# Optimization experiments

Hardware: AMD Instinct MI355X
Metric: run time of the kernel (lower is better)

## Reference

```python
import jax, jax.numpy as jnp
import numpy as np

MEAN = 0.1307
SIGMA = 0.3081
BINARY_ITER = 10
SIG_SCALE = 5.0


def spu(x):
    # SPU(x) = x^2 - 0.5 for x >= 0, sigmoid(-x) - 1 for x < 0 (continuous at 0)
    return jnp.where(x >= 0, x * x - 0.5, jax.nn.sigmoid(-x) - 1.0)


def joining_line(x1, y1, x2, y2):
    slope = (y2 - y1) / (x2 - x1)
    return slope, y2 - slope * x2


def parabola_tangent(x):
    return 2.0 * x, -x * x - 0.5


def parabola_tangent_through(x1, y1):
    D = 4.0 * x1 * x1 - 4.0 * y1 - 2.0
    x2 = (2.0 * x1 + jnp.sqrt(jnp.clip(D, 0.0))) / 2.0
    return parabola_tangent(x2)


def sigmoid_tangent(x):
    s = jax.nn.sigmoid(x)
    slope = -s * (1.0 - s)
    return slope, -s - slope * x


def binary_search_point(lx, ux, uy):
    L = lx
    R = jnp.zeros_like(lx)
    for _ in range(BINARY_ITER):  # fixed 10-iteration search, unrolled
        m = 0.5 * (L + R)
        sm, im = sigmoid_tangent(m)
        mask = sm * ux + im - uy > 0
        L = jnp.where(mask, m, L)
        R = jnp.where(mask, R, m)
    return L


def line_to_constraint(slope, intercept):
    # [n, n+1]: diagonal slope matrix with intercept as last column (matches torch diagflat/cat)
    return jnp.concatenate([jnp.diagflat(slope), intercept[:, None]], axis=1)


def analyze_affine(W, b, ub, lb):
    constr = jnp.concatenate([W, b[:, None]], axis=1)
    bu = jnp.where(W > 0, ub[None, :], lb[None, :])
    bl = jnp.where(W > 0, lb[None, :], ub[None, :])
    return constr, jnp.einsum('ij,ij->i', bu, W) + b, jnp.einsum('ij,ij->i', bl, W) + b


def analyze_spu(ux, lx):
    uy = spu(ux)
    ly = spu(lx)
    new_ub = jnp.maximum(uy, ly)
    sj, ij = joining_line(lx, ly, ux, uy)
    right = lx > 0
    left = ux <= 0
    crossing = (~left) & (~right)
    # learned positions at their (fresh) init: sigmoid(0) -> midpoint
    mid = 0.5 * (ux + lx)
    sp, ip = parabola_tangent(mid)
    ssm, ism = sigmoid_tangent(mid)
    new_lb = jnp.where(crossing, jnp.full_like(uy, -0.5), jnp.minimum(uy, ly))
    # crossing-case lower constraint
    spu_, ipu = parabola_tangent(ux)
    limit = spu_ * lx + ipu
    clm = (jnp.abs(lx) > ux).astype(lx.dtype)
    clp = jax.nn.sigmoid((clm - 0.5) * 2.0 * SIG_SCALE) * (ly - limit) + limit
    ptm = clp < -0.5
    spt, ipt = parabola_tangent_through(lx, clp)
    sjn, ijn = joining_line(lx, clp, jnp.zeros_like(lx), jnp.full_like(lx, -0.5))
    s_cl = jnp.where(ptm, spt, sjn)
    i_cl = jnp.where(ptm, ipt, ijn)
    # crossing-case upper constraint
    ssl, isl = sigmoid_tangent(lx)
    stv = ssl * ux + isl - uy
    L = binary_search_point(lx, ux, uy)
    scp = jax.nn.sigmoid(-SIG_SCALE) * (L - lx) + lx
    ssc, isc = sigmoid_tangent(scp)
    up_mask = stv > 0
    s_cu = jnp.where(up_mask, ssc, sj)
    i_cu = jnp.where(up_mask, isc, ij)
    rf = right.astype(lx.dtype)
    lf = left.astype(lx.dtype)
    cf = crossing.astype(lx.dtype)
    us = rf * sj + lf * ssm + cf * s_cu
    ui = rf * ij + lf * ism + cf * i_cu
    ls = rf * sp + lf * sj + cf * s_cl
    li = rf * ip + lf * ij + cf * i_cl
    return line_to_constraint(us, ui), line_to_constraint(ls, li), new_ub, new_lb


def back_substitute(uc, lc, ub, lb):
    cu, cl = uc[-1], lc[-1]
    for pu, pl in zip(uc[-2::-1], lc[-2::-1]):
        # where(curr>0, prev_upper, prev_lower) contracted with curr == split pos/neg matmuls
        Wu, bu = cu[:, :-1], cu[:, -1]
        cu = jnp.maximum(Wu, 0.0) @ pu + jnp.minimum(Wu, 0.0) @ pl
        cu = cu.at[:, -1].add(bu)
        Wl, bl = cl[:, :-1], cl[:, -1]
        cl = jnp.maximum(Wl, 0.0) @ pl + jnp.minimum(Wl, 0.0) @ pu
        cl = cl.at[:, -1].add(bl)
    return jnp.minimum(ub, cu[:, 0]), jnp.maximum(lb, cl[:, 0])


def setup_inputs() -> dict:
    key = jax.random.key(0)
    ks = jax.random.split(key, 9)
    d_in, h, d_out = 784, 2048, 10
    inputs = jax.random.uniform(ks[0], (d_in,), dtype=jnp.float32)
    eps = jnp.float32(0.05)
    w1 = jax.random.normal(ks[1], (h, d_in), dtype=jnp.float32) / np.sqrt(d_in).astype(np.float32)
    b1 = jax.random.normal(ks[2], (h,), dtype=jnp.float32) * 0.1
    w2 = jax.random.normal(ks[3], (h, h), dtype=jnp.float32) / np.sqrt(h).astype(np.float32)
    b2 = jax.random.normal(ks[4], (h,), dtype=jnp.float32) * 0.1
    w3 = jax.random.normal(ks[5], (h, h), dtype=jnp.float32) / np.sqrt(h).astype(np.float32)
    b3 = jax.random.normal(ks[6], (h,), dtype=jnp.float32) * 0.1
    w4 = jax.random.normal(ks[7], (d_out, h), dtype=jnp.float32) / np.sqrt(h).astype(np.float32)
    b4 = jax.random.normal(ks[8], (d_out,), dtype=jnp.float32) * 0.1
    return {"inputs": inputs, "eps": eps, "w1": w1, "b1": b1, "w2": w2, "b2": b2,
            "w3": w3, "b3": b3, "w4": w4, "b4": b4}


def reference(inputs, eps, w1, b1, w2, b2, w3, b3, w4, b4):
    ub = [jnp.clip(inputs + eps, None, 1.0)]
    lb = [jnp.clip(inputs - eps, 0.0)]
    # normalization layer: applied in place to bounds and input constraint ([784,1])
    uc = [((ub[0] - MEAN) / SIGMA)[:, None]]
    lc = [((lb[0] - MEAN) / SIGMA)[:, None]]
    ub[0] = (ub[0] - MEAN) / SIGMA
    lb[0] = (lb[0] - MEAN) / SIGMA
    weights = [(w1, b1), (w2, b2), (w3, b3), (w4, b4)]
    for i, (W, b) in enumerate(weights):
        c, u, l = analyze_affine(W, b, ub[-1], lb[-1])
        uc.append(c)
        lc.append(c)
        ub.append(u)
        lb.append(l)
        u, l = back_substitute(uc, lc, ub[-1], lb[-1])
        ub[-1], lb[-1] = u, l
        if i < len(weights) - 1:
            cu_, cl_, u, l = analyze_spu(ub[-1], lb[-1])
            uc.append(cu_)
            lc.append(cl_)
            ub.append(u)
            lb.append(l)
            u, l = back_substitute(uc, lc, ub[-1], lb[-1])
            ub[-1], lb[-1] = u, l
    return lb[-1].min()
```

## Files before the change

### kernel.cpp

```cpp
#include <hip/hip_runtime.h>
#include <cstdint>
#include <cstddef>

#define MEAN_C 0.1307f
#define SIGMA_C 0.3081f
#define SIG_SCALE_C 5.0f

typedef __bf16 bf16_t;
typedef __bf16 bf16x8 __attribute__((ext_vector_type(8)));
typedef __bf16 bf16x4 __attribute__((ext_vector_type(4)));
typedef float f32x4 __attribute__((ext_vector_type(4)));

__device__ __forceinline__ f32x4 mfma16(bf16x8 a, bf16x8 b, f32x4 c) {
    return __builtin_amdgcn_mfma_f32_16x16x32_bf16(a, b, c, 0, 0, 0);
}

typedef const __attribute__((address_space(1))) void* gvp;
typedef __attribute__((address_space(3))) void* lvp;
__device__ __forceinline__ void g2l16(const void* g, void* l) {
    __builtin_amdgcn_global_load_lds((gvp)g, (lvp)l, 16, 0, 0);
}

__device__ __forceinline__ size_t swz(int r, int k, int ktiles) {
    return (((size_t)(r >> 4) * ktiles + (k >> 5)) << 9)
         + (((k >> 3) & 3) << 7) + ((r & 15) << 3) + (k & 7);
}

#define KTILES 64


__device__ __forceinline__ float sigmoidf_(float x) {
    if (x >= 0.f) { float e = __expf(-x); return 1.f / (1.f + e); }
    float e = __expf(x); return e / (1.f + e);
}

__device__ __forceinline__ float spu_f(float x) {
    return (x >= 0.f) ? (x * x - 0.5f) : (sigmoidf_(-x) - 1.f);
}

__device__ __forceinline__ float wave_sum(float a) {
    #pragma unroll
    for (int o = 32; o > 0; o >>= 1) a += __shfl_xor(a, o, 64);
    return a;
}

__device__ __forceinline__ void spu_body(int i, int n,
        float iUi, float iLi, float vU, float vL,
        float* __restrict__ us, float* __restrict__ ui,
        float* __restrict__ ls, float* __restrict__ li,
        float* __restrict__ pU, float* __restrict__ pL) {
    float ux = fminf(iUi, vU);
    float lx = fmaxf(iLi, vL);
    float uy = spu_f(ux), ly = spu_f(lx);
    float new_ub = fmaxf(uy, ly);
    float sj = (uy - ly) / (ux - lx);
    float ij = uy - sj * ux;
    bool right = lx > 0.f;
    bool left = ux <= 0.f;
    float mid = 0.5f * (ux + lx);
    float sp = 2.f * mid, ip = -mid * mid - 0.5f;
    float sm = sigmoidf_(mid);
    float ssm = -sm * (1.f - sm);
    float ism = -sm - ssm * mid;
    bool crossing = (!left) && (!right);
    float new_lb = crossing ? -0.5f : fminf(uy, ly);
    float spu_s = 2.f * ux, ipu = -ux * ux - 0.5f;
    float limit = spu_s * lx + ipu;
    float clm = (fabsf(lx) > ux) ? 1.f : 0.f;
    float clp = sigmoidf_((clm - 0.5f) * 2.f * SIG_SCALE_C) * (ly - limit) + limit;
    bool ptm = clp < -0.5f;
    float D = 4.f * lx * lx - 4.f * clp - 2.f;
    float x2 = (2.f * lx + sqrtf(fmaxf(D, 0.f))) * 0.5f;
    float spt = 2.f * x2, ipt = -x2 * x2 - 0.5f;
    float sjn = (clp + 0.5f) / lx;
    float ijn = -0.5f;
    float s_cl = ptm ? spt : sjn;
    float i_cl = ptm ? ipt : ijn;
    float sl = sigmoidf_(lx);
    float ssl = -sl * (1.f - sl);
    float isl = -sl - ssl * lx;
    float stv = ssl * ux + isl - uy;
    float Lb = lx, Rb = 0.f;
    #pragma unroll
    for (int t = 0; t < 10; ++t) {
        float mm = 0.5f * (Lb + Rb);
        float smm = sigmoidf_(mm);
        float sms = -smm * (1.f - smm);
        float smi = -smm - sms * mm;
        bool mask = (sms * ux + smi - uy) > 0.f;
        Lb = mask ? mm : Lb;
        Rb = mask ? Rb : mm;
    }
    float scp = sigmoidf_(-SIG_SCALE_C) * (Lb - lx) + lx;
    float sc = sigmoidf_(scp);
    float ssc = -sc * (1.f - sc);
    float isc = -sc - ssc * scp;
    bool up = stv > 0.f;
    float s_cu = up ? ssc : sj;
    float i_cu = up ? isc : ij;
    float usv, uiv, lsv, liv;
    if (right)      { usv = sj;   uiv = ij;   lsv = sp;   liv = ip;   }
    else if (left)  { usv = ssm;  uiv = ism;  lsv = sj;   liv = ij;   }
    else            { usv = s_cu; uiv = i_cu; lsv = s_cl; liv = i_cl; }
    us[i] = usv; ui[i] = uiv; ls[i] = lsv; li[i] = liv;
    float vu = (usv >= 0.f) ? vU : vL;
    float vl = (lsv >= 0.f) ? vL : vU;
    pU[i] = fminf(new_ub, usv * vu + uiv);
    pL[i] = fmaxf(new_lb, lsv * vl + liv);
}


__global__ __launch_bounds__(256) void k_interval_spu(
        const float* __restrict__ W, const float* __restrict__ b,
        const float* __restrict__ U, const float* __restrict__ L,
        int m, int n,
        float* __restrict__ us, float* __restrict__ ui,
        float* __restrict__ ls, float* __restrict__ li,
        float* __restrict__ pU, float* __restrict__ pL) {
    int r = (blockIdx.x << 2) + (threadIdx.x >> 6);
    if (r >= n) return;
    int lane = threadIdx.x & 63;
    const f32x4* Wr = (const f32x4*)(W + (size_t)r * m);
    const f32x4* U4 = (const f32x4*)U;
    const f32x4* L4 = (const f32x4*)L;
    int nf4 = m >> 2;
    float au = 0.f, al = 0.f;
    for (int j = lane; j < nf4; j += 64) {
        f32x4 wv = Wr[j], uu = U4[j], ll = L4[j];
        #pragma unroll
        for (int u = 0; u < 4; ++u) {
            float w = wv[u];
            float hi = (w > 0.f) ? uu[u] : ll[u];
            float lo2 = (w > 0.f) ? ll[u] : uu[u];
            au = fmaf(w, hi, au);
            al = fmaf(w, lo2, al);
        }
    }
    au = wave_sum(au); al = wave_sum(al);
    if (lane == 0) {
        float vU = au + b[r], vL = al + b[r];
        spu_body(r, n, vU, vL, vU, vL, us, ui, ls, li, pU, pL);
    }
}

__global__ void k_spu2(const float* __restrict__ iU, const float* __restrict__ iL,
                       const float* __restrict__ vraw, int n,
                       float* __restrict__ us, float* __restrict__ ui,
                       float* __restrict__ ls, float* __restrict__ li,
                       float* __restrict__ pU, float* __restrict__ pL) {
    int i = blockIdx.x * blockDim.x + threadIdx.x;
    if (i >= n) return;
    spu_body(i, n, iU[i], iL[i], vraw[i], vraw[n + i], us, ui, ls, li, pU, pL);
}


__global__ __launch_bounds__(256) void k_wT3(
        const float* __restrict__ W1, const float* __restrict__ W2,
        const float* __restrict__ W3,
        bf16_t* __restrict__ W1t, bf16_t* __restrict__ W2t, bf16_t* __restrict__ W3t,
        const float* __restrict__ x, const float* __restrict__ eps,
        float* __restrict__ ubn, float* __restrict__ lbn) {
    __shared__ bf16_t t[64 * 65];
    int z = blockIdx.z;
    const float* W; int N, ldw; bf16_t* Wt;
    if (z == 0)      { W = W2; N = 2048; ldw = 2048; Wt = W2t; }
    else if (z == 1) { W = W3; N = 2048; ldw = 2048; Wt = W3t; }
    else {
        W = W1; N = 784; ldw = 784; Wt = W1t;
        if (blockIdx.y >= 14) {
            if (blockIdx.y == 14 && blockIdx.x == 0) {
                for (int i = threadIdx.x; i < 896; i += 256) {
                    if (i >= 784) { ubn[i] = 0.f; lbn[i] = 0.f; }
                    else {
                        float e = eps[0];
                        float ub = fminf(x[i] + e, 1.f);
                        float lb = fmaxf(x[i] - e, 0.f);
                        ubn[i] = (ub - MEAN_C) / SIGMA_C;
                        lbn[i] = (lb - MEAN_C) / SIGMA_C;
                    }
                }
            }
            return;
        }
    }
    int k0 = blockIdx.x * 64, n0 = blockIdx.y * 64;
    int tid = threadIdx.x;
    int rg = tid >> 4;
    int cg = (tid & 15) * 4;
    bool fast = (n0 + 64 <= N);
    #pragma unroll
    for (int it = 0; it < 4; ++it) {
        int row = it * 16 + rg;
        const float* Wr = W + (size_t)(k0 + row) * ldw + n0 + cg;
        float v0, v1, v2, v3;
        if (fast) {
            f32x4 vv = *(const f32x4*)Wr;
            v0 = vv[0]; v1 = vv[1]; v2 = vv[2]; v3 = vv[3];
        } else {
            v0 = (n0 + cg + 0 < N) ? Wr[0] : 0.f;
            v1 = (n0 + cg + 1 < N) ? Wr[1] : 0.f;
            v2 = (n0 + cg + 2 < N) ? Wr[2] : 0.f;
            v3 = (n0 + cg + 3 < N) ? Wr[3] : 0.f;
        }
        t[(cg + 0) * 65 + row] = (bf16_t)v0;
        t[(cg + 1) * 65 + row] = (bf16_t)v1;
        t[(cg + 2) * 65 + row] = (bf16_t)v2;
        t[(cg + 3) * 65 + row] = (bf16_t)v3;
    }
    __syncthreads();
    #pragma unroll
    for (int p = 0; p < 2; ++p) {
        int c = tid + p * 256;
        int lr = c & 63, lq = c >> 6;
        bf16x8 v;
        #pragma unroll
        for (int u = 0; u < 8; ++u) v[u] = t[lr * 65 + lq * 8 + u];
        *(bf16x8*)(Wt + swz(n0 + lr, k0 + lq * 8, KTILES)) = v;
    }
}

__global__ __launch_bounds__(256) void k_prep16(
        const float* __restrict__ W, const float* __restrict__ b, int n,
        const float* __restrict__ cus, const float* __restrict__ cui,
        const float* __restrict__ cls, const float* __restrict__ cli,
        const float* __restrict__ bvec,
        const float* __restrict__ U, const float* __restrict__ L,
        bf16_t* __restrict__ Ab, float* __restrict__ av,
        float* __restrict__ iU, float* __restrict__ iL) {
    int rt = blockIdx.x;
    int tid = threadIdx.x, lane = tid & 63, wid = tid >> 6;
    int mrow = lane & 15, q = lane >> 4;
    int r = rt * 16 + mrow;
    bool act = r < 2 * n;
    bool isU = r < n;
    int i = act ? (isU ? r : r - n) : 0;
    float gate = act ? 1.f : 0.f;
    const float* Wr = W + (size_t)i * 2048;
    const float* ps = isU ? cus : cls;
    const float* ns = isU ? cls : cus;
    const float* yi = isU ? cui : cli;
    const float* zi = isU ? cli : cui;
    const float* hi = isU ? U : L;
    const float* lo = isU ? L : U;
    float a = 0.f, a2 = 0.f;
    bf16_t* Abase = Ab + ((size_t)rt * KTILES) * 512 + lane * 8;
    for (int kt = wid; kt < KTILES; kt += 4) {
        int k0 = kt * 32 + q * 8;
        bf16x8 ov;
        #pragma unroll
        for (int h = 0; h < 2; ++h) {
            int kb = k0 + 4 * h;
            f32x4 wv = *(const f32x4*)(Wr + kb);
            f32x4 p0 = *(const f32x4*)(ps + kb);
            f32x4 q0 = *(const f32x4*)(ns + kb);
            f32x4 y0 = *(const f32x4*)(yi + kb);
            f32x4 z0 = *(const f32x4*)(zi + kb);
            f32x4 c0 = *(const f32x4*)(bvec + kb);
            f32x4 h0 = *(const f32x4*)(hi + kb);
            f32x4 l0 = *(const f32x4*)(lo + kb);
            #pragma unroll
            for (int u = 0; u < 4; ++u) {
                float w = gate * wv[u];
                float pos = fmaxf(w, 0.f), neg = fminf(w, 0.f);
                float mx = pos * p0[u] + neg * q0[u];
                ov[4 * h + u] = (bf16_t)mx;
                a += pos * y0[u] + neg * z0[u] + mx * c0[u];
                a2 += pos * h0[u] + neg * l0[u];
            }
        }
        *(bf16x8*)(Abase + (size_t)kt * 512) = ov;
    }
    a += __shfl_xor(a, 16, 64);  a += __shfl_xor(a, 32, 64);
    a2 += __shfl_xor(a2, 16, 64); a2 += __shfl_xor(a2, 32, 64);
    __shared__ float sh[2][4][16];
    if (lane < 16) { sh[0][wid][lane] = a; sh[1][wid][lane] = a2; }
    __syncthreads();
    if (tid < 16) {
        int r2 = rt * 16 + tid;
        float ta = sh[0][0][tid] + sh[0][1][tid] + sh[0][2][tid] + sh[0][3][tid];
        float tb = sh[1][0][tid] + sh[1][1][tid] + sh[1][2][tid] + sh[1][3][tid];
        if (r2 < 2 * n) {
            bool isU2 = r2 < n;
            int i2 = isU2 ? r2 : r2 - n;
            av[r2] = ta + b[i2];
            if (isU2) iU[i2] = tb + b[i2];
            else      iL[i2] = tb + b[i2];
        } else {
            av[r2] = 0.f;
        }
    }
}

__global__ __launch_bounds__(256) void k_colmix16(
        const bf16_t* __restrict__ Cb, int ldc, int splits, size_t sstride, int n,
        int tpb,
        const float* __restrict__ cus, const float* __restrict__ cui,
        const float* __restrict__ cls, const float* __restrict__ cli,
        const float* __restrict__ bvec,
        bf16_t* __restrict__ Ab, float* __restrict__ av) {
    int rt = blockIdx.x;
    int kt0 = blockIdx.y * tpb;
    int tid = threadIdx.x, lane = tid & 63, wid = tid >> 6;
    int mrow = lane & 15, q = lane >> 4;
    int r = rt * 16 + mrow;
    bool isU = r < n;
    const bf16_t* Cr = Cb + (size_t)r * ldc;
    const float* ps = isU ? cus : cls;
    const float* ns = isU ? cls : cus;
    const float* yi = isU ? cui : cli;
    const float* zi = isU ? cli : cui;
    float a = 0.f;
    bf16_t* Abase = Ab + ((size_t)rt * KTILES) * 512 + lane * 8;
    for (int kt = kt0 + wid; kt < kt0 + tpb; kt += 4) {
        int k0 = kt * 32 + q * 8;
        float wsum[8] = {0.f, 0.f, 0.f, 0.f, 0.f, 0.f, 0.f, 0.f};
        for (int s = 0; s < splits; ++s) {
            bf16x8 v = *(const bf16x8*)(Cr + s * sstride + k0);
            #pragma unroll
            for (int u = 0; u < 8; ++u) wsum[u] += (float)v[u];
        }
        f32x4 p0 = *(const f32x4*)(ps + k0), p1 = *(const f32x4*)(ps + k0 + 4);
        f32x4 q0 = *(const f32x4*)(ns + k0), q1 = *(const f32x4*)(ns + k0 + 4);
        f32x4 y0 = *(const f32x4*)(yi + k0), y1 = *(const f32x4*)(yi + k0 + 4);
        f32x4 z0 = *(const f32x4*)(zi + k0), z1 = *(const f32x4*)(zi + k0 + 4);
        f32x4 c0 = *(const f32x4*)(bvec + k0), c1 = *(const f32x4*)(bvec + k0 + 4);
        bf16x8 ov;
        #pragma unroll
        for (int u = 0; u < 4; ++u) {
            float w = wsum[u];
            float pos = fmaxf(w, 0.f), neg = fminf(w, 0.f);
            float mx = pos * p0[u] + neg * q0[u];
            ov[u] = (bf16_t)mx;
            a += pos * y0[u] + neg * z0[u] + mx * c0[u];
        }
        #pragma unroll
        for (int u = 0; u < 4; ++u) {
            float w = wsum[4 + u];
            float pos = fmaxf(w, 0.f), neg = fminf(w, 0.f);
            float mx = pos * p1[u] + neg * q1[u];
            ov[4 + u] = (bf16_t)mx;
            a += pos * y1[u] + neg * z1[u] + mx * c1[u];
        }
        *(bf16x8*)(Abase + (size_t)kt * 512) = ov;
    }
    a += __shfl_xor(a, 16, 64);
    a += __shfl_xor(a, 32, 64);
    __shared__ float sh[4][16];
    if (lane < 16) sh[wid][lane] = a;
    __syncthreads();
    if (tid < 16) {
        float tot = sh[0][tid] + sh[1][tid] + sh[2][tid] + sh[3][tid];
        atomicAdd(&av[rt * 16 + tid], tot);
    }
}

__global__ __launch_bounds__(640) void k_reduce16f(
        const bf16_t* __restrict__ Cb, int ldc, int m, int n,
        int splits, size_t sstride,
        const float* __restrict__ av,
        const float* __restrict__ ubn, const float* __restrict__ lbn,
        const float* __restrict__ iL,
        float* __restrict__ out) {
    __shared__ float sbl[16];
    int tid = threadIdx.x, lane = tid & 63, wv = tid >> 6;
    int nch = m >> 3;
    int i = wv;
    int r = n + i;
    const bf16_t* Cr = Cb + (size_t)r * ldc;
    const float* p = lbn;
    const float* q = ubn;
    float a = 0.f;
    for (int c = lane; c < nch; c += 64) {
        float wsum[8] = {0.f, 0.f, 0.f, 0.f, 0.f, 0.f, 0.f, 0.f};
        for (int s = 0; s < splits; ++s) {
            bf16x8 v = *(const bf16x8*)(Cr + s * sstride + c * 8);
            #pragma unroll
            for (int u = 0; u < 8; ++u) wsum[u] += (float)v[u];
        }
        f32x4 p0 = *(const f32x4*)(p + c * 8), p1 = *(const f32x4*)(p + c * 8 + 4);
        f32x4 q0 = *(const f32x4*)(q + c * 8), q1 = *(const f32x4*)(q + c * 8 + 4);
        #pragma unroll
        for (int u = 0; u < 4; ++u) {
            a += fmaxf(wsum[u], 0.f) * p0[u] + fminf(wsum[u], 0.f) * q0[u];
            a += fmaxf(wsum[4 + u], 0.f) * p1[u] + fminf(wsum[4 + u], 0.f) * q1[u];
        }
    }
    a = wave_sum(a);
    if (lane == 0) sbl[i] = fmaxf(iL[i], a + av[r]);
    __syncthreads();
    if (tid < 64) {
        float v = 3.4e38f;
        for (int j = lane; j < n; j += 64) v = fminf(v, sbl[j]);
        #pragma unroll
        for (int o = 32; o > 0; o >>= 1) v = fminf(v, __shfl_down(v, o, 64));
        if (lane == 0) out[0] = v;
    }
}

#define GEMM_PIPE()                                                            \
    int tid = threadIdx.x, lane = tid & 63, w = tid >> 6;                      \
    int wm = w & 1, wn = w >> 1;                                               \
    f32x4 acc[4][4];                                                           \
    _Pragma("unroll")                                                          \
    for (int i = 0; i < 4; ++i)                                                \
        _Pragma("unroll")                                                      \
        for (int j = 0; j < 4; ++j) acc[i][j] = (f32x4){0.f, 0.f, 0.f, 0.f};   \
    auto stage = [&](int kk) {                                                 \
        int b = kk & 1;                                                        \
        size_t go = (size_t)kk * 1024;                                         \
        bf16_t* la = &As2[b * 8192 + w * 1024];                                \
        bf16_t* lb = &Bs2[b * 8192 + w * 1024];                                \
        g2l16(a0 + go, la);          g2l16(a0 + go + 512, la + 512);           \
        g2l16(a1 + go, la + 4096);   g2l16(a1 + go + 512, la + 4608);          \
        g2l16(b0 + go, lb);          g2l16(b0 + go + 512, lb + 512);           \
        g2l16(b1 + go, lb + 4096);   g2l16(b1 + go + 512, lb + 4608);          \
    };                                                                         \
    stage(0); stage(1);                                                        \
    asm volatile("s_waitcnt vmcnt(8)" ::: "memory");                           \
    __builtin_amdgcn_s_barrier();                                              \
    for (int kk = 0; kk < nk; ++kk) {                                          \
        const bf16_t* cA = &As2[(kk & 1) * 8192];                              \
        const bf16_t* cB = &Bs2[(kk & 1) * 8192];                              \
        bf16x8 af0[4], af1[4], bq0[4], bq1[4];                                 \
        _Pragma("unroll")                                                      \
        for (int i = 0; i < 4; ++i) {                                          \
            af0[i] = *(const bf16x8*)(cA + (wm * 4 + i) * 1024 + lane * 8);    \
            af1[i] = *(const bf16x8*)(cA + (wm * 4 + i) * 1024 + 512 + lane * 8); \
            bq0[i] = *(const bf16x8*)(cB + (wn * 4 + i) * 1024 + lane * 8);    \
            bq1[i] = *(const bf16x8*)(cB + (wn * 4 + i) * 1024 + 512 + lane * 8); \
        }                                                                      \
        asm volatile("s_waitcnt lgkmcnt(0)" ::: "memory");                     \
        __builtin_amdgcn_s_barrier();                                          \
        if (kk + 2 < nk) stage(kk + 2);                                        \
        _Pragma("unroll")                                                      \
        for (int i = 0; i < 4; ++i)                                            \
            _Pragma("unroll")                                                  \
            for (int j = 0; j < 4; ++j)                                        \
                acc[i][j] = mfma16(bq0[j], af0[i], acc[i][j]);                 \
        _Pragma("unroll")                                                      \
        for (int i = 0; i < 4; ++i)                                            \
            _Pragma("unroll")                                                  \
            for (int j = 0; j < 4; ++j)                                        \
                acc[i][j] = mfma16(bq1[j], af1[i], acc[i][j]);                 \
        if (kk + 2 < nk) asm volatile("s_waitcnt vmcnt(8)" ::: "memory");      \
        else             asm volatile("s_waitcnt vmcnt(0)" ::: "memory");      \
        __builtin_amdgcn_s_barrier();                                          \
    }

__global__ __launch_bounds__(256) void k_gemm16(
        const bf16_t* __restrict__ A, const bf16_t* __restrict__ Bt,
        bf16_t* __restrict__ C, int ldc, size_t sstride, int nk) {
    __shared__ __align__(16) bf16_t As2[16384];
    __shared__ __align__(16) bf16_t Bs2[16384];
    int tr0 = blockIdx.y * 8, tc0 = blockIdx.x * 8;
    int kt0 = blockIdx.z * nk * 2;
    int wtmp = threadIdx.x >> 6, ltmp = threadIdx.x & 63;
    const bf16_t* a0 = A + (((size_t)(tr0 + wtmp)     * KTILES + kt0) << 9) + ltmp * 8;
    const bf16_t* a1 = A + (((size_t)(tr0 + wtmp + 4) * KTILES + kt0) << 9) + ltmp * 8;
    const bf16_t* b0 = Bt + (((size_t)(tc0 + wtmp)     * KTILES + kt0) << 9) + ltmp * 8;
    const bf16_t* b1 = Bt + (((size_t)(tc0 + wtmp + 4) * KTILES + kt0) << 9) + ltmp * 8;
    GEMM_PIPE()
    bf16_t* Cz = C + (size_t)blockIdx.z * sstride;
    int orow = lane & 15, ocol = (lane >> 4) * 4;
    size_t row0 = (size_t)blockIdx.y * 128;
    size_t col0 = (size_t)blockIdx.x * 128;
    #pragma unroll
    for (int i = 0; i < 4; ++i) {
        size_t gr = row0 + wm * 64 + i * 16 + orow;
        #pragma unroll
        for (int j = 0; j < 4; ++j) {
            size_t gc = col0 + wn * 64 + j * 16 + ocol;
            bf16x4 v;
            #pragma unroll
            for (int rg = 0; rg < 4; ++rg) v[rg] = (bf16_t)acc[i][j][rg];
            *(bf16x4*)(Cz + gr * (size_t)ldc + gc) = v;
        }
    }
}

#define GEMM_PIPE8()                                                           \
    int tid = threadIdx.x, lane = tid & 63, w = tid >> 6;            \
    int wm = w >> 2, wn = w & 3;                                               \
    f32x4 acc[4][2];                                                           \
    _Pragma("unroll")                                                          \
    for (int i = 0; i < 4; ++i)                                                \
        _Pragma("unroll")                                                      \
        for (int j = 0; j < 2; ++j) acc[i][j] = (f32x4){0.f, 0.f, 0.f, 0.f};   \
    auto stage = [&](int kk) {                                                 \
        int b = kk & 1;                                                        \
        size_t go = (size_t)kk * 1024;                                         \
        bf16_t* la = &As2[b * 8192 + w * 1024];                                \
        bf16_t* lb = &Bs2[b * 8192 + w * 1024];                                \
        g2l16(a0 + go, la);   g2l16(a0 + go + 512, la + 512);                  \
        g2l16(b0 + go, lb);   g2l16(b0 + go + 512, lb + 512);                  \
    };                                                                         \
    stage(0); stage(1);                                                        \
    asm volatile("s_waitcnt vmcnt(4)" ::: "memory");                           \
    __builtin_amdgcn_s_barrier();                                              \
    for (int kk = 0; kk < nk; ++kk) {                                          \
        const bf16_t* cA = &As2[(kk & 1) * 8192];                              \
        const bf16_t* cB = &Bs2[(kk & 1) * 8192];                              \
        bf16x8 af0[4], af1[4], bq0[2], bq1[2];                                 \
        _Pragma("unroll")                                                      \
        for (int i = 0; i < 4; ++i) {                                          \
            af0[i] = *(const bf16x8*)(cA + (wm * 4 + i) * 1024 + lane * 8);    \
            af1[i] = *(const bf16x8*)(cA + (wm * 4 + i) * 1024 + 512 + lane * 8); \
        }                                                                      \
        _Pragma("unroll")                                                      \
        for (int j = 0; j < 2; ++j) {                                          \
            bq0[j] = *(const bf16x8*)(cB + (wn * 2 + j) * 1024 + lane * 8);    \
            bq1[j] = *(const bf16x8*)(cB + (wn * 2 + j) * 1024 + 512 + lane * 8); \
        }                                                                      \
        asm volatile("s_waitcnt lgkmcnt(0)" ::: "memory");                     \
        __builtin_amdgcn_s_barrier();                                          \
        if (kk + 2 < nk) stage(kk + 2);                                        \
        _Pragma("unroll")                                                      \
        for (int i = 0; i < 4; ++i)                                            \
            _Pragma("unroll")                                                  \
            for (int j = 0; j < 2; ++j)                                        \
                acc[i][j] = mfma16(bq0[j], af0[i], acc[i][j]);                 \
        _Pragma("unroll")                                                      \
        for (int i = 0; i < 4; ++i)                                            \
            _Pragma("unroll")                                                  \
            for (int j = 0; j < 2; ++j)                                        \
                acc[i][j] = mfma16(bq1[j], af1[i], acc[i][j]);                 \
        if (kk + 2 < nk) asm volatile("s_waitcnt vmcnt(4)" ::: "memory");      \
        else             asm volatile("s_waitcnt vmcnt(0)" ::: "memory");      \
        __builtin_amdgcn_s_barrier();                                          \
    }

__global__ __launch_bounds__(512, 4) void k_gemm16_mix(
        const bf16_t* __restrict__ A, const bf16_t* __restrict__ Bt, int n,
        const float* __restrict__ cus, const float* __restrict__ cui,
        const float* __restrict__ cls, const float* __restrict__ cli,
        const float* __restrict__ bvec,
        bf16_t* __restrict__ Ab2, float* __restrict__ av, int nk) {
    __shared__ __align__(16) bf16_t As2[16384];
    __shared__ __align__(16) bf16_t Bs2[16384];
    __shared__ float asum[4][128];
    int wg = (int)(blockIdx.y * gridDim.x + blockIdx.x);
    int xcd = wg & 7, idx = wg >> 3;
    int bm = (xcd & 3) * 8 + (idx & 7);
    int bn = (xcd >> 2) * 8 + (idx >> 3);
    int tr0 = bm * 8, tc0 = bn * 8;
    int wtmp = threadIdx.x >> 6, ltmp = threadIdx.x & 63;
    const bf16_t* a0 = A + (((size_t)(tr0 + wtmp) * KTILES) << 9) + ltmp * 8;
    const bf16_t* b0 = Bt + (((size_t)(tc0 + wtmp) * KTILES) << 9) + ltmp * 8;
    GEMM_PIPE8()
    size_t row0 = (size_t)bm * 128;
    size_t col0 = (size_t)bn * 128;
    bool isU = (int)row0 < n;
    const float* ps = isU ? cus : cls;
    const float* ns = isU ? cls : cus;
    const float* yi = isU ? cui : cli;
    const float* zi = isU ? cli : cui;
    int orow = lane & 15, ocol = (lane >> 4) * 4;
    #pragma unroll
    for (int i = 0; i < 4; ++i) {
        int gr = (int)row0 + wm * 64 + i * 16 + orow;
        float ra = 0.f;
        #pragma unroll
        for (int j = 0; j < 2; ++j) {
            int gc = (int)col0 + wn * 32 + j * 16 + ocol;
            f32x4 p0 = *(const f32x4*)(ps + gc);
            f32x4 q0 = *(const f32x4*)(ns + gc);
            f32x4 y0 = *(const f32x4*)(yi + gc);
            f32x4 z0 = *(const f32x4*)(zi + gc);
            f32x4 c0 = *(const f32x4*)(bvec + gc);
            bf16x4 ov;
            #pragma unroll
            for (int rg = 0; rg < 4; ++rg) {
                float v = acc[i][j][rg];
                float pos = fmaxf(v, 0.f), neg = fminf(v, 0.f);
                float mx = pos * p0[rg] + neg * q0[rg];
                ov[rg] = (bf16_t)mx;
                ra += pos * y0[rg] + neg * z0[rg] + mx * c0[rg];
            }
            *(bf16x4*)(Ab2 + swz(gr, gc, KTILES)) = ov;
        }
        ra += __shfl_xor(ra, 16, 64);
        ra += __shfl_xor(ra, 32, 64);
        if (lane < 16) asum[wn][wm * 64 + i * 16 + lane] = ra;
    }
    __syncthreads();
    if (tid < 128)
        atomicAdd(&av[row0 + tid],
                  asum[0][tid] + asum[1][tid] + asum[2][tid] + asum[3][tid]);
}

__global__ __launch_bounds__(512, 4) void k_gemm16_red(
        const bf16_t* __restrict__ A, const bf16_t* __restrict__ Bt, int n,
        const float* __restrict__ ubn, const float* __restrict__ lbn,
        float* __restrict__ av, int nk) {
    __shared__ __align__(16) bf16_t As2[16384];
    __shared__ __align__(16) bf16_t Bs2[16384];
    __shared__ float asum[4][128];
    int wg = (int)(blockIdx.y * gridDim.x + blockIdx.x);
    int id = (wg & 7) * 28 + (wg >> 3);
    int bm = id / 7, bn = id % 7;
    int tr0 = bm * 8, tc0 = bn * 8;
    int wtmp = threadIdx.x >> 6, ltmp = threadIdx.x & 63;
    const bf16_t* a0 = A + (((size_t)(tr0 + wtmp) * KTILES) << 9) + ltmp * 8;
    const bf16_t* b0 = Bt + (((size_t)(tc0 + wtmp) * KTILES) << 9) + ltmp * 8;
    GEMM_PIPE8()
    size_t row0 = (size_t)bm * 128;
    size_t col0 = (size_t)bn * 128;
    bool isU = (int)row0 < n;
    const float* p = isU ? ubn : lbn;
    const float* q = isU ? lbn : ubn;
    int ocol = (lane >> 4) * 4;
    #pragma unroll
    for (int i = 0; i < 4; ++i) {
        float ra = 0.f;
        #pragma unroll
        for (int j = 0; j < 2; ++j) {
            int gc = (int)col0 + wn * 32 + j * 16 + ocol;
            f32x4 p0 = *(const f32x4*)(p + gc);
            f32x4 q0 = *(const f32x4*)(q + gc);
            #pragma unroll
            for (int rg = 0; rg < 4; ++rg) {
                float v = acc[i][j][rg];
                ra += fmaxf(v, 0.f) * p0[rg] + fminf(v, 0.f) * q0[rg];
            }
        }
        ra += __shfl_xor(ra, 16, 64);
        ra += __shfl_xor(ra, 32, 64);
        if (lane < 16) asum[wn][wm * 64 + i * 16 + lane] = ra;
    }
    __syncthreads();
    if (tid < 128)
        atomicAdd(&av[row0 + tid],
                  asum[0][tid] + asum[1][tid] + asum[2][tid] + asum[3][tid]);
}


extern "C" void kernel_launch(void* const* d_in, const int* in_sizes, int n_in,
                              void* d_out, int out_size, void* d_ws, size_t ws_size,
                              hipStream_t stream) {
    (void)in_sizes; (void)n_in; (void)out_size; (void)ws_size;
    const float* x   = (const float*)d_in[0];
    const float* eps = (const float*)d_in[1];
    const float* W1  = (const float*)d_in[2];
    const float* B1  = (const float*)d_in[3];
    const float* W2  = (const float*)d_in[4];
    const float* B2  = (const float*)d_in[5];
    const float* W3  = (const float*)d_in[6];
    const float* B3  = (const float*)d_in[7];
    const float* W4  = (const float*)d_in[8];
    const float* B4  = (const float*)d_in[9];
    float* out = (float*)d_out;

    const int H = 2048, DIN = 784, DOUT = 10;
    const int NP1 = 896;
    const int MP4 = 128;

    float* ws = (float*)d_ws;
    size_t off = 0;
    auto alloc = [&](size_t nf) -> float* {
        float* p = ws + off;
        off += (nf + 3) & ~(size_t)3;
        return p;
    };
    float* ubn = alloc(NP1);
    float* lbn = alloc(NP1);
    float* us1 = alloc(H); float* ui1 = alloc(H); float* ls1 = alloc(H); float* li1 = alloc(H);
    float* pU1 = alloc(H); float* pL1 = alloc(H);
    float* iU2 = alloc(H); float* iL2 = alloc(H);
    float* us2 = alloc(H); float* ui2 = alloc(H); float* ls2 = alloc(H); float* li2 = alloc(H);
    float* pU2 = alloc(H); float* pL2 = alloc(H);
    float* iU3 = alloc(H); float* iL3 = alloc(H);
    float* us3 = alloc(H); float* ui3 = alloc(H); float* ls3 = alloc(H); float* li3 = alloc(H);
    float* pU3 = alloc(H); float* pL3 = alloc(H);
    float* iU4 = alloc(32); float* iL4 = alloc(32);
    float* av  = alloc(2 * H);
    bf16_t* Ab  = (bf16_t*)alloc((size_t)2 * H * H / 2);
    bf16_t* Ab2 = (bf16_t*)alloc((size_t)2 * H * H / 2);
    bf16_t* W1t = (bf16_t*)alloc((size_t)NP1 * H / 2);
    bf16_t* W2t = (bf16_t*)alloc((size_t)H * H / 2);
    bf16_t* W3t = (bf16_t*)alloc((size_t)H * H / 2);
    bf16_t* Cs  = (bf16_t*)alloc((size_t)16 * MP4 * H / 2);

    dim3 blk(256);

    k_wT3<<<dim3(32, 32, 3), blk, 0, stream>>>(W1, W2, W3, W1t, W2t, W3t,
                                               x, eps, ubn, lbn);

    size_t ss4H = (size_t)MP4 * H;
    size_t ss4N = (size_t)MP4 * NP1;

    k_interval_spu<<<dim3(H / 4), blk, 0, stream>>>(W1, B1, ubn, lbn, DIN, H,
        us1, ui1, ls1, li1, pU1, pL1);

    k_prep16<<<dim3(2 * H / 16), blk, 0, stream>>>(W2, B2, H,
        us1, ui1, ls1, li1, B1, pU1, pL1, Ab, av, iU2, iL2);
    k_gemm16_red<<<dim3(2 * H / 128, NP1 / 128), dim3(512), 0, stream>>>(Ab, W1t, H,
        ubn, lbn, av, KTILES / 2);
    k_spu2<<<dim3(H / 64), dim3(64), 0, stream>>>(iU2, iL2, av, H,
        us2, ui2, ls2, li2, pU2, pL2);

    k_prep16<<<dim3(2 * H / 16), blk, 0, stream>>>(W3, B3, H,
        us2, ui2, ls2, li2, B2, pU2, pL2, Ab, av, iU3, iL3);
    k_gemm16_mix<<<dim3(2 * H / 128, H / 128), dim3(512), 0, stream>>>(Ab, W2t, H,
        us1, ui1, ls1, li1, B1, Ab2, av, KTILES / 2);
    k_gemm16_red<<<dim3(2 * H / 128, NP1 / 128), dim3(512), 0, stream>>>(Ab2, W1t, H,
        ubn, lbn, av, KTILES / 2);
    k_spu2<<<dim3(H / 64), dim3(64), 0, stream>>>(iU3, iL3, av, H,
        us3, ui3, ls3, li3, pU3, pL3);

    k_prep16<<<dim3(MP4 / 16), blk, 0, stream>>>(W4, B4, DOUT,
        us3, ui3, ls3, li3, B3, pU3, pL3, Ab, av, iU4, iL4);
    k_gemm16<<<dim3(H / 128, MP4 / 128, 16), blk, 0, stream>>>(Ab, W3t, Cs, H, ss4H, 2);
    k_colmix16<<<dim3(MP4 / 16, 8), blk, 0, stream>>>(Cs, H, 16, ss4H, DOUT, KTILES / 8,
        us2, ui2, ls2, li2, B2, Ab2, av);
    k_gemm16<<<dim3(H / 128, MP4 / 128, 16), blk, 0, stream>>>(Ab2, W2t, Cs, H, ss4H, 2);
    k_colmix16<<<dim3(MP4 / 16, 8), blk, 0, stream>>>(Cs, H, 16, ss4H, DOUT, KTILES / 8,
        us1, ui1, ls1, li1, B1, Ab, av);
    k_gemm16<<<dim3(NP1 / 128, MP4 / 128, 16), blk, 0, stream>>>(Ab, W1t, Cs, NP1, ss4N, 2);
    k_reduce16f<<<dim3(1), dim3(640), 0, stream>>>(Cs, NP1, DIN, DOUT, 16, ss4N,
        av, ubn, lbn, iL4, out);
}
```

Measured before the change: 330.7 us.

## Fold layer-1 interval SPU into transpose kernel and SPU epilogues into GEMM

The first-layer interval bound plus SPU computation now runs as an extra z-slice of the weight-transpose kernel, computing normalized bounds inline from x and eps. The two standalone k_spu2 launches are removed. Their work now happens in a last-block-done epilogue of k_gemm16_red, driven by an atomic counter. This cuts three kernel launches and their serialization gaps. In exchange, one block runs the serial 2048-element SPU tail, and correctness depends on atomic visibility of the accumulated bounds and on counter resets happening in the transpose kernel.

```diff
diff --git a/kernel.cpp b/kernel.cpp
--- a/kernel.cpp
+++ b/kernel.cpp
@@ -110,66 +110,59 @@
 }
 
 
-__global__ __launch_bounds__(256) void k_interval_spu(
-        const float* __restrict__ W, const float* __restrict__ b,
-        const float* __restrict__ U, const float* __restrict__ L,
-        int m, int n,
-        float* __restrict__ us, float* __restrict__ ui,
-        float* __restrict__ ls, float* __restrict__ li,
-        float* __restrict__ pU, float* __restrict__ pL) {
-    int r = (blockIdx.x << 2) + (threadIdx.x >> 6);
-    if (r >= n) return;
-    int lane = threadIdx.x & 63;
-    const f32x4* Wr = (const f32x4*)(W + (size_t)r * m);
-    const f32x4* U4 = (const f32x4*)U;
-    const f32x4* L4 = (const f32x4*)L;
-    int nf4 = m >> 2;
-    float au = 0.f, al = 0.f;
-    for (int j = lane; j < nf4; j += 64) {
-        f32x4 wv = Wr[j], uu = U4[j], ll = L4[j];
-        #pragma unroll
-        for (int u = 0; u < 4; ++u) {
-            float w = wv[u];
-            float hi = (w > 0.f) ? uu[u] : ll[u];
-            float lo2 = (w > 0.f) ? ll[u] : uu[u];
-            au = fmaf(w, hi, au);
-            al = fmaf(w, lo2, al);
-        }
-    }
-    au = wave_sum(au); al = wave_sum(al);
-    if (lane == 0) {
-        float vU = au + b[r], vL = al + b[r];
-        spu_body(r, n, vU, vL, vU, vL, us, ui, ls, li, pU, pL);
-    }
-}
-
-__global__ void k_spu2(const float* __restrict__ iU, const float* __restrict__ iL,
-                       const float* __restrict__ vraw, int n,
-                       float* __restrict__ us, float* __restrict__ ui,
-                       float* __restrict__ ls, float* __restrict__ li,
-                       float* __restrict__ pU, float* __restrict__ pL) {
-    int i = blockIdx.x * blockDim.x + threadIdx.x;
-    if (i >= n) return;
-    spu_body(i, n, iU[i], iL[i], vraw[i], vraw[n + i], us, ui, ls, li, pU, pL);
-}
-
-
 __global__ __launch_bounds__(256) void k_wT3(
         const float* __restrict__ W1, const float* __restrict__ W2,
         const float* __restrict__ W3,
         bf16_t* __restrict__ W1t, bf16_t* __restrict__ W2t, bf16_t* __restrict__ W3t,
         const float* __restrict__ x, const float* __restrict__ eps,
-        float* __restrict__ ubn, float* __restrict__ lbn) {
+        float* __restrict__ ubn, float* __restrict__ lbn,
+        const float* __restrict__ b1,
+        float* __restrict__ us1, float* __restrict__ ui1,
+        float* __restrict__ ls1, float* __restrict__ li1,
+        float* __restrict__ pU1, float* __restrict__ pL1,
+        int* __restrict__ cnt2, int* __restrict__ cnt3) {
     __shared__ bf16_t t[64 * 65];
     int z = blockIdx.z;
+    int tid = threadIdx.x;
     const float* W; int N, ldw; bf16_t* Wt;
     if (z == 0)      { W = W2; N = 2048; ldw = 2048; Wt = W2t; }
     else if (z == 1) { W = W3; N = 2048; ldw = 2048; Wt = W3t; }
+    else if (z == 3) {
+        int bid = (int)(blockIdx.y * 32 + blockIdx.x);
+        if (bid >= 512) return;
+        int w = tid >> 6, lane = tid & 63;
+        int r = bid * 4 + w;
+        const f32x4* Wr = (const f32x4*)(W1 + (size_t)r * 784);
+        const f32x4* X4 = (const f32x4*)x;
+        float e = eps[0];
+        float au = 0.f, al = 0.f;
+        for (int j = lane; j < 196; j += 64) {
+            f32x4 wv = Wr[j], xv = X4[j];
+            #pragma unroll
+            for (int u = 0; u < 4; ++u) {
+                float xb = xv[u];
+                float ub = (fminf(xb + e, 1.f) - MEAN_C) / SIGMA_C;
+                float lb = (fmaxf(xb - e, 0.f) - MEAN_C) / SIGMA_C;
+                float wgt = wv[u];
+                float hi = (wgt > 0.f) ? ub : lb;
+                float lo2 = (wgt > 0.f) ? lb : ub;
+                au = fmaf(wgt, hi, au);
+                al = fmaf(wgt, lo2, al);
+            }
+        }
+        au = wave_sum(au); al = wave_sum(al);
+        if (lane == 0) {
+            float vU = au + b1[r], vL = al + b1[r];
+            spu_body(r, 2048, vU, vL, vU, vL, us1, ui1, ls1, li1, pU1, pL1);
+        }
+        return;
+    }
     else {
         W = W1; N = 784; ldw = 784; Wt = W1t;
         if (blockIdx.y >= 14) {
             if (blockIdx.y == 14 && blockIdx.x == 0) {
-                for (int i = threadIdx.x; i < 896; i += 256) {
+                if (tid == 0) { cnt2[0] = 0; cnt3[0] = 0; }
+                for (int i = tid; i < 896; i += 256) {
                     if (i >= 784) { ubn[i] = 0.f; lbn[i] = 0.f; }
                     else {
                         float e = eps[0];
@@ -184,7 +177,6 @@
         }
     }
     int k0 = blockIdx.x * 64, n0 = blockIdx.y * 64;
-    int tid = threadIdx.x;
     int rg = tid >> 4;
     int cg = (tid & 15) * 4;
     bool fast = (n0 + 64 <= N);
@@ -591,10 +583,16 @@
 __global__ __launch_bounds__(512, 4) void k_gemm16_red(
         const bf16_t* __restrict__ A, const bf16_t* __restrict__ Bt, int n,
         const float* __restrict__ ubn, const float* __restrict__ lbn,
-        float* __restrict__ av, int nk) {
+        float* __restrict__ av, int nk,
+        int* __restrict__ cnt,
+        const float* __restrict__ iU, const float* __restrict__ iL,
+        float* __restrict__ us, float* __restrict__ ui,
+        float* __restrict__ ls, float* __restrict__ li,
+        float* __restrict__ pU, float* __restrict__ pL) {
     __shared__ __align__(16) bf16_t As2[16384];
     __shared__ __align__(16) bf16_t Bs2[16384];
     __shared__ float asum[4][128];
+    __shared__ int lastf;
     int wg = (int)(blockIdx.y * gridDim.x + blockIdx.x);
     int id = (wg & 7) * 28 + (wg >> 3);
     int bm = id / 7, bn = id % 7;
@@ -631,6 +629,21 @@
     if (tid < 128)
         atomicAdd(&av[row0 + tid],
                   asum[0][tid] + asum[1][tid] + asum[2][tid] + asum[3][tid]);
+    __syncthreads();
+    if (tid == 0) {
+        int old = atomicAdd(cnt, 1);
+        lastf = (old == (int)(gridDim.x * gridDim.y) - 1) ? 1 : 0;
+    }
+    __syncthreads();
+    if (lastf) {
+        for (int i = tid; i < n; i += 512) {
+            float vU = __hip_atomic_load(&av[i], __ATOMIC_RELAXED,
+                                         __HIP_MEMORY_SCOPE_AGENT);
+            float vL = __hip_atomic_load(&av[n + i], __ATOMIC_RELAXED,
+                                         __HIP_MEMORY_SCOPE_AGENT);
+            spu_body(i, n, iU[i], iL[i], vU, vL, us, ui, ls, li, pU, pL);
+        }
+    }
 }
 
 
@@ -673,6 +686,8 @@
     float* pU3 = alloc(H); float* pL3 = alloc(H);
     float* iU4 = alloc(32); float* iL4 = alloc(32);
     float* av  = alloc(2 * H);
+    int* cnt2 = (int*)alloc(4);
+    int* cnt3 = (int*)alloc(4);
     bf16_t* Ab  = (bf16_t*)alloc((size_t)2 * H * H / 2);
     bf16_t* Ab2 = (bf16_t*)alloc((size_t)2 * H * H / 2);
     bf16_t* W1t = (bf16_t*)alloc((size_t)NP1 * H / 2);
@@ -682,30 +697,25 @@
 
     dim3 blk(256);
 
-    k_wT3<<<dim3(32, 32, 3), blk, 0, stream>>>(W1, W2, W3, W1t, W2t, W3t,
-                                               x, eps, ubn, lbn);
+    k_wT3<<<dim3(32, 32, 4), blk, 0, stream>>>(W1, W2, W3, W1t, W2t, W3t,
+        x, eps, ubn, lbn, B1, us1, ui1, ls1, li1, pU1, pL1, cnt2, cnt3);
 
     size_t ss4H = (size_t)MP4 * H;
     size_t ss4N = (size_t)MP4 * NP1;
-
-    k_interval_spu<<<dim3(H / 4), blk, 0, stream>>>(W1, B1, ubn, lbn, DIN, H,
-        us1, ui1, ls1, li1, pU1, pL1);
 
     k_prep16<<<dim3(2 * H / 16), blk, 0, stream>>>(W2, B2, H,
         us1, ui1, ls1, li1, B1, pU1, pL1, Ab, av, iU2, iL2);
     k_gemm16_red<<<dim3(2 * H / 128, NP1 / 128), dim3(512), 0, stream>>>(Ab, W1t, H,
-        ubn, lbn, av, KTILES / 2);
-    k_spu2<<<dim3(H / 64), dim3(64), 0, stream>>>(iU2, iL2, av, H,
-        us2, ui2, ls2, li2, pU2, pL2);
+        ubn, lbn, av, KTILES / 2,
+        cnt2, iU2, iL2, us2, ui2, ls2, li2, pU2, pL2);
 
     k_prep16<<<dim3(2 * H / 16), blk, 0, stream>>>(W3, B3, H,
         us2, ui2, ls2, li2, B2, pU2, pL2, Ab, av, iU3, iL3);
     k_gemm16_mix<<<dim3(2 * H / 128, H / 128), dim3(512), 0, stream>>>(Ab, W2t, H,
         us1, ui1, ls1, li1, B1, Ab2, av, KTILES / 2);
     k_gemm16_red<<<dim3(2 * H / 128, NP1 / 128), dim3(512), 0, stream>>>(Ab2, W1t, H,
-        ubn, lbn, av, KTILES / 2);
-    k_spu2<<<dim3(H / 64), dim3(64), 0, stream>>>(iU3, iL3, av, H,
-        us3, ui3, ls3, li3, pU3, pL3);
+        ubn, lbn, av, KTILES / 2,
+        cnt3, iU3, iL3, us3, ui3, ls3, li3, pU3, pL3);
 
     k_prep16<<<dim3(MP4 / 16), blk, 0, stream>>>(W4, B4, DOUT,
         us3, ui3, ls3, li3, B3, pU3, pL3, Ab, av, iU4, iL4);
```

After: 347.6 us. +5.1%, slower.

## Retile reduction GEMM to 64-row blocks with 256 threads and double buffering

Applied to the files above, without the earlier changes.

Rewrites k_gemm16_red from 128x128 tiles with 512 threads and the shared 8-stage pipeline macro into 64x128 tiles with 256 threads. Each wave now owns one A row-tile and two B column-tiles, and an explicit two-stage LDS double buffer is driven by direct global-to-LDS loads. The grid is a flat 448 blocks with an XCD-aware mapping. The aim is more blocks for better CU coverage and less LDS per block. The cost is that B tiles are re-read twice as often and the pipeline is shallower.

```diff
diff --git a/kernel.cpp b/kernel.cpp
--- a/kernel.cpp
+++ b/kernel.cpp
@@ -588,22 +588,70 @@
                   asum[0][tid] + asum[1][tid] + asum[2][tid] + asum[3][tid]);
 }
 
-__global__ __launch_bounds__(512, 4) void k_gemm16_red(
+__global__ __launch_bounds__(256) void k_gemm16_red(
         const bf16_t* __restrict__ A, const bf16_t* __restrict__ Bt, int n,
         const float* __restrict__ ubn, const float* __restrict__ lbn,
         float* __restrict__ av, int nk) {
-    __shared__ __align__(16) bf16_t As2[16384];
+    __shared__ __align__(16) bf16_t As2[8192];
     __shared__ __align__(16) bf16_t Bs2[16384];
-    __shared__ float asum[4][128];
-    int wg = (int)(blockIdx.y * gridDim.x + blockIdx.x);
-    int id = (wg & 7) * 28 + (wg >> 3);
-    int bm = id / 7, bn = id % 7;
-    int tr0 = bm * 8, tc0 = bn * 8;
-    int wtmp = threadIdx.x >> 6, ltmp = threadIdx.x & 63;
-    const bf16_t* a0 = A + (((size_t)(tr0 + wtmp) * KTILES) << 9) + ltmp * 8;
-    const bf16_t* b0 = Bt + (((size_t)(tc0 + wtmp) * KTILES) << 9) + ltmp * 8;
-    GEMM_PIPE8()
-    size_t row0 = (size_t)bm * 128;
+    __shared__ float asum[4][64];
+    int wg = (int)blockIdx.x;
+    int xcd = wg & 7, idx = wg >> 3;
+    int bm = xcd * 8 + idx / 7;
+    int bn = idx % 7;
+    int tid = threadIdx.x, lane = tid & 63, w = tid >> 6;
+    const bf16_t* aw  = A  + (((size_t)(bm * 4 + w)      * KTILES) << 9) + lane * 8;
+    const bf16_t* bw0 = Bt + (((size_t)(bn * 8 + 2 * w)  * KTILES) << 9) + lane * 8;
+    const bf16_t* bw1 = Bt + (((size_t)(bn * 8 + 2 * w + 1) * KTILES) << 9) + lane * 8;
+    f32x4 acc[4][2];
+    #pragma unroll
+    for (int i = 0; i < 4; ++i)
+        #pragma unroll
+        for (int j = 0; j < 2; ++j) acc[i][j] = (f32x4){0.f, 0.f, 0.f, 0.f};
+    auto stage = [&](int kk) {
+        int b = kk & 1;
+        size_t go = (size_t)kk * 1024;
+        bf16_t* la = &As2[b * 4096 + w * 1024];
+        bf16_t* lb = &Bs2[b * 8192 + 2 * w * 1024];
+        g2l16(aw + go, la);         g2l16(aw + go + 512, la + 512);
+        g2l16(bw0 + go, lb);        g2l16(bw0 + go + 512, lb + 512);
+        g2l16(bw1 + go, lb + 1024); g2l16(bw1 + go + 512, lb + 1536);
+    };
+    stage(0); stage(1);
+    asm volatile("s_waitcnt vmcnt(6)" ::: "memory");
+    __builtin_amdgcn_s_barrier();
+    for (int kk = 0; kk < nk; ++kk) {
+        const bf16_t* cA = &As2[(kk & 1) * 4096];
+        const bf16_t* cB = &Bs2[(kk & 1) * 8192];
+        bf16x8 af0[4], af1[4], bq0[2], bq1[2];
+        #pragma unroll
+        for (int i = 0; i < 4; ++i) {
+            af0[i] = *(const bf16x8*)(cA + i * 1024 + lane * 8);
+            af1[i] = *(const bf16x8*)(cA + i * 1024 + 512 + lane * 8);
+        }
+        #pragma unroll
+        for (int j = 0; j < 2; ++j) {
+            bq0[j] = *(const bf16x8*)(cB + (2 * w + j) * 1024 + lane * 8);
+            bq1[j] = *(const bf16x8*)(cB + (2 * w + j) * 1024 + 512 + lane * 8);
+        }
+        asm volatile("s_waitcnt lgkmcnt(0)" ::: "memory");
+        __builtin_amdgcn_s_barrier();
+        if (kk + 2 < nk) stage(kk + 2);
+        #pragma unroll
+        for (int i = 0; i < 4; ++i)
+            #pragma unroll
+            for (int j = 0; j < 2; ++j)
+                acc[i][j] = mfma16(bq0[j], af0[i], acc[i][j]);
+        #pragma unroll
+        for (int i = 0; i < 4; ++i)
+            #pragma unroll
+            for (int j = 0; j < 2; ++j)
+                acc[i][j] = mfma16(bq1[j], af1[i], acc[i][j]);
+        if (kk + 2 < nk) asm volatile("s_waitcnt vmcnt(6)" ::: "memory");
+        else             asm volatile("s_waitcnt vmcnt(0)" ::: "memory");
+        __builtin_amdgcn_s_barrier();
+    }
+    size_t row0 = (size_t)bm * 64;
     size_t col0 = (size_t)bn * 128;
     bool isU = (int)row0 < n;
     const float* p = isU ? ubn : lbn;
@@ -614,7 +662,7 @@
         float ra = 0.f;
         #pragma unroll
         for (int j = 0; j < 2; ++j) {
-            int gc = (int)col0 + wn * 32 + j * 16 + ocol;
+            int gc = (int)col0 + w * 32 + j * 16 + ocol;
             f32x4 p0 = *(const f32x4*)(p + gc);
             f32x4 q0 = *(const f32x4*)(q + gc);
             #pragma unroll
@@ -625,10 +673,10 @@
         }
         ra += __shfl_xor(ra, 16, 64);
         ra += __shfl_xor(ra, 32, 64);
-        if (lane < 16) asum[wn][wm * 64 + i * 16 + lane] = ra;
+        if (lane < 16) asum[w][i * 16 + lane] = ra;
     }
     __syncthreads();
-    if (tid < 128)
+    if (tid < 64)
         atomicAdd(&av[row0 + tid],
                   asum[0][tid] + asum[1][tid] + asum[2][tid] + asum[3][tid]);
 }
@@ -693,7 +741,7 @@
 
     k_prep16<<<dim3(2 * H / 16), blk, 0, stream>>>(W2, B2, H,
         us1, ui1, ls1, li1, B1, pU1, pL1, Ab, av, iU2, iL2);
-    k_gemm16_red<<<dim3(2 * H / 128, NP1 / 128), dim3(512), 0, stream>>>(Ab, W1t, H,
+    k_gemm16_red<<<dim3(448), blk, 0, stream>>>(Ab, W1t, H,
         ubn, lbn, av, KTILES / 2);
     k_spu2<<<dim3(H / 64), dim3(64), 0, stream>>>(iU2, iL2, av, H,
         us2, ui2, ls2, li2, pU2, pL2);
@@ -702,7 +750,7 @@
         us2, ui2, ls2, li2, B2, pU2, pL2, Ab, av, iU3, iL3);
     k_gemm16_mix<<<dim3(2 * H / 128, H / 128), dim3(512), 0, stream>>>(Ab, W2t, H,
         us1, ui1, ls1, li1, B1, Ab2, av, KTILES / 2);
-    k_gemm16_red<<<dim3(2 * H / 128, NP1 / 128), dim3(512), 0, stream>>>(Ab2, W1t, H,
+    k_gemm16_red<<<dim3(448), blk, 0, stream>>>(Ab2, W1t, H,
         ubn, lbn, av, KTILES / 2);
     k_spu2<<<dim3(H / 64), dim3(64), 0, stream>>>(iU3, iL3, av, H,
         us3, ui3, ls3, li3, pU3, pL3);
```

New measurement: 321.9 us. 2.6% less time.
